# Kernel optimization log

Measured on AMD Instinct MI355X. Metric: run time of the kernel, lower is better.

The kernel has to match this reference:

```python
import jax, jax.numpy as jnp
import numpy as np

N_NODES = 100000
N_EDGES = 600000
DIM = 128
NUM_CLASSES = 10
NUM_GRAPHS = 512
NUM_LAYERS = 4
BN_EPS = 1e-5


def _bn(h, g, b):
    # BatchNorm1d, training-mode statistics (biased variance), affine
    m = h.mean(axis=0)
    v = jnp.var(h, axis=0)
    return (h - m) * jax.lax.rsqrt(v + BN_EPS) * g + b


def setup_inputs() -> dict:
    key = jax.random.key(0)
    ks = jax.random.split(key, 8)
    s_in = 1.0 / np.sqrt(DIM)
    x = jax.random.normal(ks[0], (N_NODES, DIM), dtype=jnp.float32)
    edge_index = jax.random.randint(ks[1], (2, N_EDGES), 0, N_NODES, dtype=jnp.int32)
    batch = jnp.sort(jax.random.randint(ks[2], (N_NODES,), 0, NUM_GRAPHS, dtype=jnp.int32))
    return {
        "x": x,
        "edge_index": edge_index,
        "batch": batch,
        "mlp_w1": jax.random.normal(ks[3], (NUM_LAYERS, DIM, DIM), dtype=jnp.float32) * s_in,
        "mlp_b1": jnp.zeros((NUM_LAYERS, DIM), dtype=jnp.float32),
        "mlp_bn_g": jnp.ones((NUM_LAYERS, DIM), dtype=jnp.float32),
        "mlp_bn_b": jnp.zeros((NUM_LAYERS, DIM), dtype=jnp.float32),
        "mlp_w2": jax.random.normal(ks[4], (NUM_LAYERS, DIM, DIM), dtype=jnp.float32) * s_in,
        "mlp_b2": jnp.zeros((NUM_LAYERS, DIM), dtype=jnp.float32),
        "bn_g": jnp.ones((NUM_LAYERS, DIM), dtype=jnp.float32),
        "bn_b": jnp.zeros((NUM_LAYERS, DIM), dtype=jnp.float32),
        "fc_w": jax.random.normal(ks[5], (NUM_LAYERS + 1, DIM, NUM_CLASSES), dtype=jnp.float32) * s_in,
        "fc_b": jnp.zeros((NUM_LAYERS + 1, NUM_CLASSES), dtype=jnp.float32),
    }


def reference(x, edge_index, batch, mlp_w1, mlp_b1, mlp_bn_g, mlp_bn_b,
              mlp_w2, mlp_b2, bn_g, bn_b, fc_w, fc_b):
    src, dst = edge_index[0], edge_index[1]
    outs = [x]
    h = x
    for i in range(NUM_LAYERS):
        # GINConv: (1+eps)*x + sum_{j in N(i)} x_j  with eps=0 (default)
        agg = jax.ops.segment_sum(h[src], dst, num_segments=N_NODES)
        z = h + agg
        # nn.Sequential(Linear, BatchNorm1d, ReLU, Linear)
        z = jax.nn.relu(_bn(z @ mlp_w1[i] + mlp_b1[i], mlp_bn_g[i], mlp_bn_b[i]))
        z = z @ mlp_w2[i] + mlp_b2[i]
        # outer BN + ReLU
        h = jax.nn.relu(_bn(z, bn_g[i], bn_b[i]))
        outs.append(h)
    out = None
    for i, o in enumerate(outs):
        pooled = jax.ops.segment_sum(o, batch, num_segments=NUM_GRAPHS)
        y = pooled @ fc_w[i] + fc_b[i]  # dropout is identity in eval mode
        out = y if out is None else out + y
    return jax.nn.log_softmax(out, axis=-1)
```

## Files before the change

### kernel.cpp

```cpp
#include <hip/hip_runtime.h>

#define NN 100000
#define NE 600000
#define DD 128
#define NG 512
#define NC 10
#define NL 4

typedef __attribute__((ext_vector_type(8))) short short8;
typedef __attribute__((ext_vector_type(4))) float f32x4;

__device__ __forceinline__ float b2f(unsigned int u) { return __uint_as_float(u << 16); }
__device__ __forceinline__ unsigned int f2b(float f) {
    unsigned int u = __float_as_uint(f);
    return (u + 0x7fffu + ((u >> 16) & 1u)) >> 16;
}
__device__ __forceinline__ void unpack8(uint4 v, float* f) {
    f[0] = b2f(v.x & 0xffffu); f[1] = b2f(v.x >> 16);
    f[2] = b2f(v.y & 0xffffu); f[3] = b2f(v.y >> 16);
    f[4] = b2f(v.z & 0xffffu); f[5] = b2f(v.z >> 16);
    f[6] = b2f(v.w & 0xffffu); f[7] = b2f(v.w >> 16);
}
__device__ __forceinline__ uint4 pack8(const float* f) {
    uint4 v;
    v.x = f2b(f[0]) | (f2b(f[1]) << 16);
    v.y = f2b(f[2]) | (f2b(f[3]) << 16);
    v.z = f2b(f[4]) | (f2b(f[5]) << 16);
    v.w = f2b(f[6]) | (f2b(f[7]) << 16);
    return v;
}

__device__ __forceinline__ void gload_lds16(const void* g, void* l) {
    __builtin_amdgcn_global_load_lds((__attribute__((address_space(1))) void*)g,
                                     (__attribute__((address_space(3))) void*)l, 16, 0, 0);
}

__device__ __forceinline__ void build_bnp(const float* __restrict__ st, const float* __restrict__ gma,
                                          const float* __restrict__ bta, float (*bnp)[DD], int t) {
    if (t < DD) {
        float s = 0.f, q = 0.f;
        #pragma unroll
        for (int r = 0; r < 8; ++r) { s += st[r * DD + t]; q += st[8 * DD + r * DD + t]; }
        const float invn = 1.0f / NN;
        float m = s * invn;
        float var = q * invn - m * m;
        float sc = gma[t] * rsqrtf(var + 1e-5f);
        bnp[0][t] = sc;
        bnp[1][t] = bta[t] - m * sc;
    }
}


__global__ __launch_bounds__(256) void k_zero(float* __restrict__ p, int n) {
    int i = blockIdx.x * 256 + threadIdx.x;
    if (i < n) p[i] = 0.f;
}
__global__ __launch_bounds__(256) void k_zeroint(int* __restrict__ p, int n) {
    int i = blockIdx.x * 256 + threadIdx.x;
    if (i < n) p[i] = 0;
}
__global__ __launch_bounds__(256) void k_copyint(const int* __restrict__ s, int* __restrict__ d, int n) {
    int i = blockIdx.x * 256 + threadIdx.x;
    if (i < n) d[i] = s[i];
}

__global__ __launch_bounds__(256) void k_cvtH(const float* __restrict__ x, ushort* __restrict__ h) {
    int i = blockIdx.x * 256 + threadIdx.x;
    if (i >= NN * DD / 8) return;
    float4 a = ((const float4*)x)[2 * i], b = ((const float4*)x)[2 * i + 1];
    float f[8] = {a.x, a.y, a.z, a.w, b.x, b.y, b.z, b.w};
    ((uint4*)h)[i] = pack8(f);
}

__global__ __launch_bounds__(256) void k_wpack(const float* __restrict__ w1, const float* __restrict__ w2,
                                               ushort* __restrict__ wp) {
    int id = blockIdx.x * 256 + threadIdx.x;
    int v = id & 63;
    int kc = (id >> 6) & 3;
    int ct = (id >> 8) & 7;
    int m = id >> 11;
    const float* W = (m < 4) ? (w1 + (size_t)m * DD * DD) : (w2 + (size_t)(m - 4) * DD * DD);
    int c = ct * 16 + (v & 15);
    int kbase = kc * 32 + ((v >> 4) << 3);
    ushort* dst = wp + ((size_t)id << 3);
    #pragma unroll
    for (int j = 0; j < 8; ++j) dst[j] = (ushort)f2b(W[(size_t)(kbase + j) * DD + c]);
}


__global__ __launch_bounds__(256) void k_hist(const int* __restrict__ dst, int* __restrict__ deg) {
    int e = blockIdx.x * 256 + threadIdx.x;
    if (e < NE) atomicAdd(&deg[dst[e]], 1);
}
__global__ __launch_bounds__(256) void k_partial(const int* __restrict__ deg, int* __restrict__ part) {
    __shared__ int s[256];
    int t = threadIdx.x;
    int i = blockIdx.x * 256 + t;
    s[t] = (i < NN) ? deg[i] : 0;
    __syncthreads();
    #pragma unroll
    for (int off = 128; off >= 1; off >>= 1) {
        if (t < off) s[t] += s[t + off];
        __syncthreads();
    }
    if (t == 0) part[blockIdx.x] = s[0];
}
__global__ __launch_bounds__(512) void k_scanpart(int* __restrict__ part, int nb) {
    __shared__ int s[512];
    int t = threadIdx.x;
    int v = (t < nb) ? part[t] : 0;
    s[t] = v;
    __syncthreads();
    #pragma unroll
    for (int off = 1; off < 512; off <<= 1) {
        int add = (t >= off) ? s[t - off] : 0;
        __syncthreads();
        s[t] += add;
        __syncthreads();
    }
    if (t < nb) part[t] = s[t] - v;
}
__global__ __launch_bounds__(256) void k_exscan(const int* __restrict__ deg, const int* __restrict__ part,
                                                int* __restrict__ rowofs) {
    __shared__ int s[256];
    int b = blockIdx.x, t = threadIdx.x;
    int i = b * 256 + t;
    int v = (i < NN) ? deg[i] : 0;
    s[t] = v;
    __syncthreads();
    #pragma unroll
    for (int off = 1; off < 256; off <<= 1) {
        int add = (t >= off) ? s[t - off] : 0;
        __syncthreads();
        s[t] += add;
        __syncthreads();
    }
    if (i < NN) rowofs[i] = part[b] + s[t] - v;
    if (i == NN - 1) rowofs[NN] = part[b] + s[t];
}
__global__ __launch_bounds__(256) void k_fill(const int* __restrict__ src, const int* __restrict__ dst,
                                              int* __restrict__ cursor, int* __restrict__ csr) {
    int e = blockIdx.x * 256 + threadIdx.x;
    if (e >= NE) return;
    int d = dst[e];
    int pos = atomicAdd(&cursor[d], 1);
    csr[pos] = src[e];
}

template<bool BN>
__global__ __launch_bounds__(256) void k_gather(const int* __restrict__ rowofs, const int* __restrict__ csr,
                                                const int* __restrict__ batch,
                                                const ushort* __restrict__ h, ushort* __restrict__ z,
                                                const float* __restrict__ st, const float* __restrict__ gma,
                                                const float* __restrict__ bta,
                                                float* __restrict__ poolslot) {
    __shared__ float bnp[2][DD];
    __shared__ float sfl[16][DD];
    __shared__ int gids[16];
    int t = threadIdx.x;
    if (BN) build_bnp(st, gma, bta, bnp, t);
    int rs = t >> 4;
    int n = blockIdx.x * 16 + rs;
    int cl = t & 15;
    int cb = cl * 8;
    if (cl == 0) gids[rs] = batch[n];
    if (BN) __syncthreads();
    float sc[8], sh[8];
    if (BN) {
        #pragma unroll
        for (int j = 0; j < 8; ++j) { sc[j] = bnp[0][cb + j]; sh[j] = bnp[1][cb + j]; }
    }
    float acc[8], f[8];
    uint4 v = ((const uint4*)h)[(size_t)n * 16 + cl];
    unpack8(v, f);
    #pragma unroll
    for (int j = 0; j < 8; ++j)
        acc[j] = BN ? fmaxf(fmaf(f[j], sc[j], sh[j]), 0.f) : f[j];
    #pragma unroll
    for (int j = 0; j < 8; j += 4)
        *(float4*)(&sfl[rs][cb + j]) = make_float4(acc[j], acc[j + 1], acc[j + 2], acc[j + 3]);
    __syncthreads();
    if (t < DD) {
        float run = sfl[0][t];
        int gprev = gids[0];
        #pragma unroll
        for (int s = 1; s < 16; ++s) {
            int gg = gids[s];
            float vv = sfl[s][t];
            if (gg != gprev) {
                atomicAdd(poolslot + (size_t)gprev * DD + t, run);
                run = 0.f;
                gprev = gg;
            }
            run += vv;
        }
        atomicAdd(poolslot + (size_t)gprev * DD + t, run);
    }
    int e = rowofs[n], end = rowofs[n + 1];
    for (; e + 1 < end; e += 2) {
        int s0 = csr[e], s1 = csr[e + 1];
        uint4 v0 = ((const uint4*)h)[(size_t)s0 * 16 + cl];
        uint4 v1 = ((const uint4*)h)[(size_t)s1 * 16 + cl];
        float f0[8], f1[8];
        unpack8(v0, f0);
        unpack8(v1, f1);
        #pragma unroll
        for (int j = 0; j < 8; ++j) {
            float a0 = BN ? fmaxf(fmaf(f0[j], sc[j], sh[j]), 0.f) : f0[j];
            float a1 = BN ? fmaxf(fmaf(f1[j], sc[j], sh[j]), 0.f) : f1[j];
            acc[j] += a0 + a1;
        }
    }
    if (e < end) {
        int s0 = csr[e];
        uint4 v0 = ((const uint4*)h)[(size_t)s0 * 16 + cl];
        float f0[8];
        unpack8(v0, f0);
        #pragma unroll
        for (int j = 0; j < 8; ++j)
            acc[j] += BN ? fmaxf(fmaf(f0[j], sc[j], sh[j]), 0.f) : f0[j];
    }
    ((uint4*)z)[(size_t)n * 16 + cl] = pack8(acc);
}

template<bool TRANS>
__global__ __launch_bounds__(256, 4) void k_mm(const ushort* __restrict__ in, const ushort* __restrict__ wp,
                                               const float* __restrict__ bias,
                                               const float* __restrict__ stin, const float* __restrict__ gma,
                                               const float* __restrict__ bta,
                                               ushort* __restrict__ outp, float* __restrict__ stout) {
    __shared__ __align__(16) char lds[16384];
    __shared__ float bnp[2][DD];
    const int t = threadIdx.x;
    const int lane = t & 63;
    const int wid = t >> 6;
    const int wr = wid >> 1, wc = wid & 1;
    const int rb = blockIdx.x * 64;
    const int rep = blockIdx.x & 7;

    if (TRANS) {
        build_bnp(stin, gma, bta, bnp, t);
        __syncthreads();
    }
    if (!TRANS && rb + 64 <= NN) {
        #pragma unroll
        for (int i = 0; i < 4; ++i) {
            int p = i * 256 + t;
            int row = p >> 4;
            int oc = (p & 15) ^ (row & 7);
            gload_lds16((const uint4*)in + (size_t)(rb + row) * 16 + oc, lds + p * 16);
        }
    } else {
        float scv[8], shv[8];
        if (TRANS) {
            int cb = (t & 15) * 8;
            #pragma unroll
            for (int j = 0; j < 8; ++j) { scv[j] = bnp[0][cb + j]; shv[j] = bnp[1][cb + j]; }
        }
        #pragma unroll
        for (int i = 0; i < 4; ++i) {
            int c = i * 256 + t;
            int row = c >> 4;
            int g = rb + row;
            uint4 v = make_uint4(0, 0, 0, 0);
            if (g < NN) {
                v = *((const uint4*)in + (size_t)g * 16 + (c & 15));
                if (TRANS) {
                    float f[8];
                    unpack8(v, f);
                    #pragma unroll
                    for (int j = 0; j < 8; ++j) f[j] = fmaxf(fmaf(f[j], scv[j], shv[j]), 0.f);
                    v = pack8(f);
                }
            }
            *(uint4*)(lds + ((c * 16) ^ ((row & 7) << 4))) = v;
        }
    }
    __syncthreads();

    f32x4 acc[2][4];
    #pragma unroll
    for (int rt = 0; rt < 2; ++rt)
        #pragma unroll
        for (int ct = 0; ct < 4; ++ct) acc[rt][ct] = (f32x4){0.f, 0.f, 0.f, 0.f};

    #pragma unroll
    for (int kc = 0; kc < 4; ++kc) {
        short8 wf[4];
        #pragma unroll
        for (int ct = 0; ct < 4; ++ct)
            wf[ct] = *(const short8*)(wp + (size_t)((((wc * 4 + ct) * 4 + kc) * 64 + lane) << 3));
        #pragma unroll
        for (int rt = 0; rt < 2; ++rt) {
            int row = wr * 32 + rt * 16 + (lane & 15);
            int off = (row * 256 + ((kc * 32 + ((lane >> 4) << 3)) << 1)) ^ ((row & 7) << 4);
            short8 zf = *(const short8*)(lds + off);
            #pragma unroll
            for (int ct = 0; ct < 4; ++ct)
                acc[rt][ct] = __builtin_amdgcn_mfma_f32_16x16x32_bf16(wf[ct], zf, acc[rt][ct], 0, 0, 0);
        }
    }
    __syncthreads();

    const int zr = lane & 15, cq = lane >> 4;
    #pragma unroll
    for (int rt = 0; rt < 2; ++rt) {
        int row = wr * 32 + rt * 16 + zr;
        #pragma unroll
        for (int ct = 0; ct < 4; ++ct) {
            int c0 = wc * 64 + ct * 16 + cq * 4;
            float4 bi = *(const float4*)(bias + c0);
            f32x4 a = acc[rt][ct];
            uint2 pk;
            pk.x = f2b(a[0] + bi.x) | (f2b(a[1] + bi.y) << 16);
            pk.y = f2b(a[2] + bi.z) | (f2b(a[3] + bi.w) << 16);
            *(uint2*)(lds + ((row * 256 + c0 * 2) ^ ((row & 7) << 4))) = pk;
        }
    }
    __syncthreads();

    float s8[8], q8[8];
    #pragma unroll
    for (int j = 0; j < 8; ++j) { s8[j] = 0.f; q8[j] = 0.f; }
    #pragma unroll
    for (int i = 0; i < 4; ++i) {
        int c = i * 256 + t;
        int row = c >> 4;
        int g = rb + row;
        if (g < NN) {
            uint4 v = *(const uint4*)(lds + ((c * 16) ^ ((row & 7) << 4)));
            ((uint4*)outp)[(size_t)g * 16 + (c & 15)] = v;
            float f[8];
            unpack8(v, f);
            #pragma unroll
            for (int j = 0; j < 8; ++j) { s8[j] += f[j]; q8[j] += f[j] * f[j]; }
        }
    }
    __syncthreads();
    float* rs = (float*)lds;
    float* rq = rs + 16 * DD;
    const int slot = t >> 4, cb2 = (t & 15) * 8;
    #pragma unroll
    for (int j = 0; j < 8; j += 4) {
        *(float4*)(rs + slot * DD + cb2 + j) = make_float4(s8[j], s8[j + 1], s8[j + 2], s8[j + 3]);
        *(float4*)(rq + slot * DD + cb2 + j) = make_float4(q8[j], q8[j + 1], q8[j + 2], q8[j + 3]);
    }
    __syncthreads();
    #pragma unroll
    for (int off = 8; off >= 1; off >>= 1) {
        if (slot < off) {
            #pragma unroll
            for (int j = 0; j < 8; j += 4) {
                float4 a = *(float4*)(rs + slot * DD + cb2 + j);
                float4 b = *(float4*)(rs + (slot + off) * DD + cb2 + j);
                a.x += b.x; a.y += b.y; a.z += b.z; a.w += b.w;
                *(float4*)(rs + slot * DD + cb2 + j) = a;
                float4 c2 = *(float4*)(rq + slot * DD + cb2 + j);
                float4 d  = *(float4*)(rq + (slot + off) * DD + cb2 + j);
                c2.x += d.x; c2.y += d.y; c2.z += d.z; c2.w += d.w;
                *(float4*)(rq + slot * DD + cb2 + j) = c2;
            }
        }
        __syncthreads();
    }
    if (t < DD) {
        atomicAdd(stout + rep * DD + t, rs[t]);
        atomicAdd(stout + 8 * DD + rep * DD + t, rq[t]);
    }
}

__device__ __forceinline__ int lowerb(const int* __restrict__ a, int n, int key) {
    int lo = 0, hi = n;
    while (lo < hi) {
        int mid = (lo + hi) >> 1;
        if (a[mid] < key) lo = mid + 1; else hi = mid;
    }
    return lo;
}

__global__ __launch_bounds__(256) void k_pool(const int* __restrict__ batch, const ushort* __restrict__ h,
                                              float* __restrict__ pooled,
                                              const float* __restrict__ st, const float* __restrict__ gma,
                                              const float* __restrict__ bta) {
    __shared__ float bnp[2][DD];
    int t = threadIdx.x;
    build_bnp(st, gma, bta, bnp, t);
    __syncthreads();
    int g = blockIdx.x;
    int cl = t & 15;
    int rs = t >> 4;
    int cb = cl * 8;
    float sc[8], sh[8];
    #pragma unroll
    for (int j = 0; j < 8; ++j) { sc[j] = bnp[0][cb + j]; sh[j] = bnp[1][cb + j]; }
    int start = lowerb(batch, NN, g);
    int end = lowerb(batch, NN, g + 1);
    float acc[8];
    #pragma unroll
    for (int j = 0; j < 8; ++j) acc[j] = 0.f;
    for (int n = start + rs; n < end; n += 16) {
        uint4 v = ((const uint4*)h)[(size_t)n * 16 + cl];
        float f[8];
        unpack8(v, f);
        #pragma unroll
        for (int j = 0; j < 8; ++j)
            acc[j] += fmaxf(fmaf(f[j], sc[j], sh[j]), 0.f);
    }
    __shared__ float red[16 * DD];
    #pragma unroll
    for (int j = 0; j < 8; j += 4)
        *(float4*)(red + rs * DD + cb + j) = make_float4(acc[j], acc[j + 1], acc[j + 2], acc[j + 3]);
    __syncthreads();
    #pragma unroll
    for (int off = 8; off >= 1; off >>= 1) {
        if (rs < off) {
            #pragma unroll
            for (int j = 0; j < 8; j += 4) {
                float4 a = *(float4*)(red + rs * DD + cb + j);
                float4 b = *(float4*)(red + (rs + off) * DD + cb + j);
                a.x += b.x; a.y += b.y; a.z += b.z; a.w += b.w;
                *(float4*)(red + rs * DD + cb + j) = a;
            }
        }
        __syncthreads();
    }
    if (rs == 0) {
        #pragma unroll
        for (int j = 0; j < 8; j += 4)
            *(float4*)(pooled + (size_t)g * DD + cb + j) = *(float4*)(red + cb + j);
    }
}

__global__ __launch_bounds__(64) void k_readout(const float* __restrict__ pooled, const float* __restrict__ fcw,
                                                const float* __restrict__ fcb, float* __restrict__ out) {
    int g = blockIdx.x, t = threadIdx.x;
    float part[NC];
    #pragma unroll
    for (int c = 0; c < NC; ++c) part[c] = 0.f;
    for (int i = 0; i < NL + 1; ++i) {
        #pragma unroll
        for (int hh = 0; hh < 2; ++hh) {
            int d = t + (hh << 6);
            float v = pooled[((size_t)i * NG + g) * DD + d];
            const float* wr = fcw + ((size_t)i * DD + d) * NC;
            #pragma unroll
            for (int c = 0; c < NC; ++c) part[c] = fmaf(v, wr[c], part[c]);
        }
    }
    #pragma unroll
    for (int off = 32; off >= 1; off >>= 1) {
        #pragma unroll
        for (int c = 0; c < NC; ++c) part[c] += __shfl_down(part[c], off);
    }
    if (t == 0) {
        float y[NC];
        #pragma unroll
        for (int c = 0; c < NC; ++c) {
            float bs = 0.f;
            for (int i = 0; i < NL + 1; ++i) bs += fcb[i * NC + c];
            y[c] = part[c] + bs;
        }
        float m = y[0];
        #pragma unroll
        for (int c = 1; c < NC; ++c) m = fmaxf(m, y[c]);
        float sum = 0.f;
        #pragma unroll
        for (int c = 0; c < NC; ++c) sum += expf(y[c] - m);
        float ls = logf(sum);
        #pragma unroll
        for (int c = 0; c < NC; ++c) out[(size_t)g * NC + c] = y[c] - m - ls;
    }
}


extern "C" void kernel_launch(void* const* d_in, const int* in_sizes, int n_in,
                              void* d_out, int out_size, void* d_ws, size_t ws_size,
                              hipStream_t stream) {
    const float* x   = (const float*)d_in[0];
    const int*   ei  = (const int*)d_in[1];
    const int*   bat = (const int*)d_in[2];
    const float* w1  = (const float*)d_in[3];
    const float* b1  = (const float*)d_in[4];
    const float* mbg = (const float*)d_in[5];
    const float* mbb = (const float*)d_in[6];
    const float* w2  = (const float*)d_in[7];
    const float* b2  = (const float*)d_in[8];
    const float* bng = (const float*)d_in[9];
    const float* bnb = (const float*)d_in[10];
    const float* fcw = (const float*)d_in[11];
    const float* fcb = (const float*)d_in[12];
    float* out = (float*)d_out;

    ushort* H  = (ushort*)d_ws;
    ushort* Z  = H + (size_t)NN * DD;
    ushort* Y1 = Z + (size_t)NN * DD;
    ushort* WP = Y1 + (size_t)NN * DD;
    float* pooled = (float*)(WP + 8 * 16384);
    float* stats  = pooled + (size_t)(NL + 1) * NG * DD;
    int* deg    = (int*)(stats + 8 * 16 * DD);
    int* rowofs = deg + NN;
    int* part   = rowofs + NN + 1;
    int* cursor = part + 512;
    int* csr    = cursor + NN;

    const int* src = ei;
    const int* dst = ei + NE;
    const int nbN = (NN + 255) / 256;
    const int nbE = (NE + 255) / 256;
    const int nzero = (NL + 1) * NG * DD + 8 * 16 * DD;

    hipLaunchKernelGGL(k_cvtH, dim3(NN * DD / 8 / 256 + 1), dim3(256), 0, stream, x, H);
    hipLaunchKernelGGL(k_zero, dim3((nzero + 255) / 256), dim3(256), 0, stream, pooled, nzero);
    hipLaunchKernelGGL(k_zeroint, dim3(nbN), dim3(256), 0, stream, deg, NN);
    hipLaunchKernelGGL(k_hist, dim3(nbE), dim3(256), 0, stream, dst, deg);
    hipLaunchKernelGGL(k_partial, dim3(nbN), dim3(256), 0, stream, deg, part);
    hipLaunchKernelGGL(k_scanpart, dim3(1), dim3(512), 0, stream, part, nbN);
    hipLaunchKernelGGL(k_exscan, dim3(nbN), dim3(256), 0, stream, deg, part, rowofs);
    hipLaunchKernelGGL(k_copyint, dim3(nbN), dim3(256), 0, stream, rowofs, cursor, NN);
    hipLaunchKernelGGL(k_fill, dim3(nbE), dim3(256), 0, stream, src, dst, cursor, csr);
    hipLaunchKernelGGL(k_wpack, dim3(64), dim3(256), 0, stream, w1, w2, WP);

    const int gmm = (NN + 63) / 64;
    const int SLOT = 16 * DD;
    for (int i = 0; i < NL; ++i) {
        float* st_mlp = stats + (size_t)(2 * i + 0) * SLOT;
        float* st_out = stats + (size_t)(2 * i + 1) * SLOT;
        const float* st_prev = stats + (size_t)(2 * i - 1) * SLOT;
        float* poolslot = pooled + (size_t)i * NG * DD;
        if (i == 0) {
            hipLaunchKernelGGL((k_gather<false>), dim3(NN / 16), dim3(256), 0, stream, rowofs, csr, bat, H, Z,
                               (const float*)nullptr, (const float*)nullptr, (const float*)nullptr, poolslot);
        } else {
            hipLaunchKernelGGL((k_gather<true>), dim3(NN / 16), dim3(256), 0, stream, rowofs, csr, bat, H, Z,
                               st_prev, bng + (size_t)(i - 1) * DD, bnb + (size_t)(i - 1) * DD, poolslot);
        }
        hipLaunchKernelGGL((k_mm<false>), dim3(gmm), dim3(256), 0, stream,
                           Z, WP + (size_t)i * 16384, b1 + (size_t)i * DD,
                           (const float*)nullptr, (const float*)nullptr, (const float*)nullptr,
                           Y1, st_mlp);
        hipLaunchKernelGGL((k_mm<true>), dim3(gmm), dim3(256), 0, stream,
                           Y1, WP + (size_t)(4 + i) * 16384, b2 + (size_t)i * DD,
                           st_mlp, mbg + (size_t)i * DD, mbb + (size_t)i * DD,
                           H, st_out);
    }
    hipLaunchKernelGGL(k_pool, dim3(NG), dim3(256), 0, stream, bat, H,
                       pooled + (size_t)NL * NG * DD,
                       stats + (size_t)7 * SLOT, bng + (size_t)3 * DD, bnb + (size_t)3 * DD);
    hipLaunchKernelGGL(k_readout, dim3(NG), dim3(64), 0, stream, pooled, fcw, fcb, out);
}
```

Measured before the change: 381.4 us.

## Fuse setup kernels and prefetch neighbor rows in gather before block sync

Measured after the change: 387.4 us. Within noise of the previous version (+1.6%).

```diff
diff --git a/kernel.cpp b/kernel.cpp
--- a/kernel.cpp
+++ b/kernel.cpp
@@ -50,41 +50,31 @@
     }
 }
 
-
-__global__ __launch_bounds__(256) void k_zero(float* __restrict__ p, int n) {
-    int i = blockIdx.x * 256 + threadIdx.x;
-    if (i < n) p[i] = 0.f;
-}
-__global__ __launch_bounds__(256) void k_zeroint(int* __restrict__ p, int n) {
-    int i = blockIdx.x * 256 + threadIdx.x;
-    if (i < n) p[i] = 0;
-}
-__global__ __launch_bounds__(256) void k_copyint(const int* __restrict__ s, int* __restrict__ d, int n) {
-    int i = blockIdx.x * 256 + threadIdx.x;
-    if (i < n) d[i] = s[i];
-}
-
-__global__ __launch_bounds__(256) void k_cvtH(const float* __restrict__ x, ushort* __restrict__ h) {
-    int i = blockIdx.x * 256 + threadIdx.x;
-    if (i >= NN * DD / 8) return;
-    float4 a = ((const float4*)x)[2 * i], b = ((const float4*)x)[2 * i + 1];
-    float f[8] = {a.x, a.y, a.z, a.w, b.x, b.y, b.z, b.w};
-    ((uint4*)h)[i] = pack8(f);
-}
-
-__global__ __launch_bounds__(256) void k_wpack(const float* __restrict__ w1, const float* __restrict__ w2,
-                                               ushort* __restrict__ wp) {
-    int id = blockIdx.x * 256 + threadIdx.x;
-    int v = id & 63;
-    int kc = (id >> 6) & 3;
-    int ct = (id >> 8) & 7;
-    int m = id >> 11;
-    const float* W = (m < 4) ? (w1 + (size_t)m * DD * DD) : (w2 + (size_t)(m - 4) * DD * DD);
-    int c = ct * 16 + (v & 15);
-    int kbase = kc * 32 + ((v >> 4) << 3);
-    ushort* dst = wp + ((size_t)id << 3);
-    #pragma unroll
-    for (int j = 0; j < 8; ++j) dst[j] = (ushort)f2b(W[(size_t)(kbase + j) * DD + c]);
+__global__ __launch_bounds__(256) void k_init(const float* __restrict__ x, ushort* __restrict__ h,
+                                              float* __restrict__ pz, int nz, int* __restrict__ deg,
+                                              const float* __restrict__ w1, const float* __restrict__ w2,
+                                              ushort* __restrict__ wp) {
+    const int T = gridDim.x * 256;
+    const int tid = blockIdx.x * 256 + threadIdx.x;
+    for (int i = tid; i < NN * DD / 8; i += T) {
+        float4 a = ((const float4*)x)[2 * i], b = ((const float4*)x)[2 * i + 1];
+        float f[8] = {a.x, a.y, a.z, a.w, b.x, b.y, b.z, b.w};
+        ((uint4*)h)[i] = pack8(f);
+    }
+    for (int i = tid; i < nz; i += T) pz[i] = 0.f;
+    for (int i = tid; i < NN; i += T) deg[i] = 0;
+    for (int id = tid; id < 16384; id += T) {
+        int v = id & 63;
+        int kc = (id >> 6) & 3;
+        int ct = (id >> 8) & 7;
+        int m = id >> 11;
+        const float* W = (m < 4) ? (w1 + (size_t)m * DD * DD) : (w2 + (size_t)(m - 4) * DD * DD);
+        int c = ct * 16 + (v & 15);
+        int kbase = kc * 32 + ((v >> 4) << 3);
+        ushort* dst = wp + ((size_t)id << 3);
+        #pragma unroll
+        for (int j = 0; j < 8; ++j) dst[j] = (ushort)f2b(W[(size_t)(kbase + j) * DD + c]);
+    }
 }
 
 
@@ -121,7 +111,7 @@
     if (t < nb) part[t] = s[t] - v;
 }
 __global__ __launch_bounds__(256) void k_exscan(const int* __restrict__ deg, const int* __restrict__ part,
-                                                int* __restrict__ rowofs) {
+                                                int* __restrict__ rowofs, int* __restrict__ cursor) {
     __shared__ int s[256];
     int b = blockIdx.x, t = threadIdx.x;
     int i = b * 256 + t;
@@ -135,7 +125,11 @@
         s[t] += add;
         __syncthreads();
     }
-    if (i < NN) rowofs[i] = part[b] + s[t] - v;
+    if (i < NN) {
+        int r = part[b] + s[t] - v;
+        rowofs[i] = r;
+        cursor[i] = r;
+    }
     if (i == NN - 1) rowofs[NN] = part[b] + s[t];
 }
 __global__ __launch_bounds__(256) void k_fill(const int* __restrict__ src, const int* __restrict__ dst,
@@ -164,6 +158,7 @@
     int cl = t & 15;
     int cb = cl * 8;
     if (cl == 0) gids[rs] = batch[n];
+    uint4 v = ((const uint4*)h)[(size_t)n * 16 + cl];
     if (BN) __syncthreads();
     float sc[8], sh[8];
     if (BN) {
@@ -171,7 +166,6 @@
         for (int j = 0; j < 8; ++j) { sc[j] = bnp[0][cb + j]; sh[j] = bnp[1][cb + j]; }
     }
     float acc[8], f[8];
-    uint4 v = ((const uint4*)h)[(size_t)n * 16 + cl];
     unpack8(v, f);
     #pragma unroll
     for (int j = 0; j < 8; ++j)
@@ -179,6 +173,12 @@
     #pragma unroll
     for (int j = 0; j < 8; j += 4)
         *(float4*)(&sfl[rs][cb + j]) = make_float4(acc[j], acc[j + 1], acc[j + 2], acc[j + 3]);
+    int e = rowofs[n], end = rowofs[n + 1];
+    const int pc = min(end - e, 4);
+    uint4 pv[4];
+    #pragma unroll
+    for (int k = 0; k < 4; ++k)
+        if (k < pc) pv[k] = ((const uint4*)h)[(size_t)csr[e + k] * 16 + cl];
     __syncthreads();
     if (t < DD) {
         float run = sfl[0][t];
@@ -196,24 +196,35 @@
         }
         atomicAdd(poolslot + (size_t)gprev * DD + t, run);
     }
-    int e = rowofs[n], end = rowofs[n + 1];
-    for (; e + 1 < end; e += 2) {
-        int s0 = csr[e], s1 = csr[e + 1];
+    #pragma unroll
+    for (int k = 0; k < 4; ++k) {
+        if (k < pc) {
+            unpack8(pv[k], f);
+            #pragma unroll
+            for (int j = 0; j < 8; ++j)
+                acc[j] += BN ? fmaxf(fmaf(f[j], sc[j], sh[j]), 0.f) : f[j];
+        }
+    }
+    e += pc;
+    for (; e + 3 < end; e += 4) {
+        int s0 = csr[e], s1 = csr[e + 1], s2 = csr[e + 2], s3 = csr[e + 3];
         uint4 v0 = ((const uint4*)h)[(size_t)s0 * 16 + cl];
         uint4 v1 = ((const uint4*)h)[(size_t)s1 * 16 + cl];
-        float f0[8], f1[8];
-        unpack8(v0, f0);
-        unpack8(v1, f1);
+        uint4 v2 = ((const uint4*)h)[(size_t)s2 * 16 + cl];
+        uint4 v3 = ((const uint4*)h)[(size_t)s3 * 16 + cl];
+        float f0[8], f1[8], f2[8], f3[8];
+        unpack8(v0, f0); unpack8(v1, f1); unpack8(v2, f2); unpack8(v3, f3);
         #pragma unroll
         for (int j = 0; j < 8; ++j) {
             float a0 = BN ? fmaxf(fmaf(f0[j], sc[j], sh[j]), 0.f) : f0[j];
             float a1 = BN ? fmaxf(fmaf(f1[j], sc[j], sh[j]), 0.f) : f1[j];
-            acc[j] += a0 + a1;
-        }
-    }
-    if (e < end) {
-        int s0 = csr[e];
-        uint4 v0 = ((const uint4*)h)[(size_t)s0 * 16 + cl];
+            float a2 = BN ? fmaxf(fmaf(f2[j], sc[j], sh[j]), 0.f) : f2[j];
+            float a3 = BN ? fmaxf(fmaf(f3[j], sc[j], sh[j]), 0.f) : f3[j];
+            acc[j] += (a0 + a1) + (a2 + a3);
+        }
+    }
+    for (; e < end; ++e) {
+        uint4 v0 = ((const uint4*)h)[(size_t)csr[e] * 16 + cl];
         float f0[8];
         unpack8(v0, f0);
         #pragma unroll
@@ -509,16 +520,13 @@
     const int nbE = (NE + 255) / 256;
     const int nzero = (NL + 1) * NG * DD + 8 * 16 * DD;
 
-    hipLaunchKernelGGL(k_cvtH, dim3(NN * DD / 8 / 256 + 1), dim3(256), 0, stream, x, H);
-    hipLaunchKernelGGL(k_zero, dim3((nzero + 255) / 256), dim3(256), 0, stream, pooled, nzero);
-    hipLaunchKernelGGL(k_zeroint, dim3(nbN), dim3(256), 0, stream, deg, NN);
+    hipLaunchKernelGGL(k_init, dim3(NN * DD / 8 / 256 + 1), dim3(256), 0, stream,
+                       x, H, pooled, nzero, deg, w1, w2, WP);
     hipLaunchKernelGGL(k_hist, dim3(nbE), dim3(256), 0, stream, dst, deg);
     hipLaunchKernelGGL(k_partial, dim3(nbN), dim3(256), 0, stream, deg, part);
     hipLaunchKernelGGL(k_scanpart, dim3(1), dim3(512), 0, stream, part, nbN);
-    hipLaunchKernelGGL(k_exscan, dim3(nbN), dim3(256), 0, stream, deg, part, rowofs);
-    hipLaunchKernelGGL(k_copyint, dim3(nbN), dim3(256), 0, stream, rowofs, cursor, NN);
+    hipLaunchKernelGGL(k_exscan, dim3(nbN), dim3(256), 0, stream, deg, part, rowofs, cursor);
     hipLaunchKernelGGL(k_fill, dim3(nbE), dim3(256), 0, stream, src, dst, cursor, csr);
-    hipLaunchKernelGGL(k_wpack, dim3(64), dim3(256), 0, stream, w1, w2, WP);
 
     const int gmm = (NN + 63) / 64;
     const int SLOT = 16 * DD;
```
